# Optimization experiments

Measured on AMD Instinct MI355X. Metric: run time of the kernel, lower is better.

The kernel has to match this reference:

```python
import jax, jax.numpy as jnp
import numpy as np

B, T, N = 512, 1024, 48


def setup_inputs() -> dict:
    key = jax.random.key(0)
    k1, k2, k3, k4 = jax.random.split(key, 4)
    potentials = jax.random.normal(k1, (B, T, N), dtype=jnp.float32)
    y_true = jax.random.randint(k2, (B, T), 0, N, dtype=jnp.int32)
    lengths = jax.random.randint(k3, (B,), 1, T + 1, dtype=jnp.int32)
    transitions = jax.random.normal(k4, (N, N), dtype=jnp.float32)
    return {"potentials": potentials, "y_true": y_true,
            "lengths": lengths, "transitions": transitions}


def _crf_log_likelihood(potentials, tags, lengths, trans):
    # potentials: [B,T,N], tags: [B,T] int, lengths: [B] int, trans: [N,N]
    Bv, Tv, Nv = potentials.shape
    t_idx = jnp.arange(Tv)

    # ---- numerator: score of the given tag sequence ----
    unary = jnp.take_along_axis(potentials, tags[..., None], axis=2)[..., 0]  # [B,T]
    unary_mask = (t_idx[None, :] < lengths[:, None]).astype(potentials.dtype)
    unary_score = jnp.sum(unary * unary_mask, axis=1)  # [B]

    trans_scores = trans[tags[:, :-1], tags[:, 1:]]  # [B,T-1]
    pair_mask = (t_idx[None, 1:] < lengths[:, None]).astype(potentials.dtype)
    binary_score = jnp.sum(trans_scores * pair_mask, axis=1)  # [B]
    seq_score = unary_score + binary_score

    # ---- log partition: forward algorithm with length masking ----
    alpha0 = potentials[:, 0, :]  # [B,N]
    pots_rest = jnp.transpose(potentials[:, 1:, :], (1, 0, 2))  # [T-1,B,N]
    valid = (t_idx[1:, None] < lengths[None, :])  # [T-1,B]

    def step(alpha, inp):
        pot_t, v = inp  # [B,N], [B]
        # logsumexp over previous state: alpha[b,i] + trans[i,j]
        new_alpha = jax.nn.logsumexp(alpha[:, :, None] + trans[None, :, :], axis=1) + pot_t
        alpha = jnp.where(v[:, None], new_alpha, alpha)
        return alpha, None

    alpha_final, _ = jax.lax.scan(step, alpha0, (pots_rest, valid))
    log_norm = jax.nn.logsumexp(alpha_final, axis=-1)  # [B]

    return seq_score - log_norm


def reference(potentials, y_true, lengths, transitions):
    ll = _crf_log_likelihood(potentials, y_true.astype(jnp.int32),
                             lengths.astype(jnp.int32), transitions)
    return -ll  # per-sample NLL, shape [B]
```

## Files before the change

kernel.cpp:

```cpp
#include <hip/hip_runtime.h>
#include <cstdint>
#include <cstddef>

constexpr int Bb = 512;
constexpr int Tt = 1024;
constexpr int Nn = 48;
constexpr int SG = 16;
constexpr int NG = Bb / SG;
constexpr int Cc = 16;
constexpr int Lc = Tt / Cc;
constexpr int Wb = 32;
constexpr int AP = 72;

typedef short bf16x8 __attribute__((ext_vector_type(8)));
typedef float f32x4  __attribute__((ext_vector_type(4)));

__device__ __forceinline__ unsigned short bf16_rne(float x) {
    const unsigned int u = __float_as_uint(x);
    return (unsigned short)((u + 0x7FFFu + ((u >> 16) & 1u)) >> 16);
}
__device__ __forceinline__ float safe_log(float x) {
    return __logf(fmaxf(x, 1e-30f));
}

__launch_bounds__(64)
__global__ void crf_fused(const float* __restrict__ pot,
                          const int*   __restrict__ ytrue,
                          const int*   __restrict__ lengths,
                          const float* __restrict__ trans,
                          float*       __restrict__ out)
{
    __shared__ float trans_lds[Nn * Nn];
    __shared__ __align__(16) unsigned short ab[SG][AP];

    const int lane = threadIdx.x;
    const int ln   = lane & 15;
    const int q    = lane >> 4;
    const int gidx = blockIdx.x >> 4;
    const int c    = blockIdx.x & 15;
    const int s0   = gidx * SG;

    for (int i = lane; i < Nn * Nn; i += 64) trans_lds[i] = trans[i];
    for (int i = lane; i < SG * AP; i += 64) ((unsigned short*)ab)[i] = 0;
    __syncthreads();

    {
        const int    b    = blockIdx.x;
        const int    lenb = lengths[b];
        const int*   yrow = ytrue + (size_t)b * Tt;
        const float* prow = pot + (size_t)b * Tt * Nn;
        float gold = 0.0f;
#pragma unroll
        for (int k = 0; k < Tt / 64; ++k) {
            const int   t    = lane + 64 * k;
            const int   yt   = yrow[t];
            const int   ytm1 = yrow[(t > 0) ? (t - 1) : 0];
            const float u    = prow[(size_t)t * Nn + yt];
            const float tr   = trans_lds[ytm1 * Nn + yt];
            gold += (t < lenb) ? u : 0.0f;
            gold += (t >= 1 && t < lenb) ? tr : 0.0f;
        }
#pragma unroll
        for (int off = 32; off > 0; off >>= 1) gold += __shfl_xor(gold, off);
        if (lane == 0) atomicAdd(&out[b], -gold);
    }

    int len4[4];
#pragma unroll
    for (int r = 0; r < 4; ++r) len4[r] = lengths[s0 + q * 4 + r];
    int lmax = lengths[s0 + ln];
#pragma unroll
    for (int off = 8; off > 0; off >>= 1) {
        const int o = __shfl_xor(lmax, off);
        lmax = (o > lmax) ? o : lmax;
    }

    const int start = (c == 0) ? 1 : c * Lc;
    if (c > 0 && start >= lmax) return;
    const int end = ((c + 1) * Lc < lmax) ? (c + 1) * Lc : lmax;

    bf16x8 Bf[3][2];
#pragma unroll
    for (int nt = 0; nt < 3; ++nt)
#pragma unroll
        for (int kc = 0; kc < 2; ++kc)
#pragma unroll
            for (int d = 0; d < 8; ++d) {
                const int i = kc * 32 + q * 8 + d;
                const int j = nt * 16 + ln;
                const float v = (i < Nn) ? __expf(trans_lds[i * Nn + j]) : 0.0f;
                Bf[nt][kc][d] = (short)bf16_rne(v);
            }

    const float* pbase[4];
#pragma unroll
    for (int r = 0; r < 4; ++r)
        pbase[r] = pot + (size_t)(s0 + q * 4 + r) * (Tt * Nn) + ln;

    const int t0 = (c == 0) ? 1 : (start - Wb);

    float pinit[3][4];
#pragma unroll
    for (int nt = 0; nt < 3; ++nt)
#pragma unroll
        for (int r = 0; r < 4; ++r)
            pinit[nt][r] = pbase[r][(size_t)(t0 - 1) * Nn + nt * 16];

    float sh4[4];
#pragma unroll
    for (int r = 0; r < 4; ++r) sh4[r] = __shfl(pinit[0][r], lane & 48);

    float prev[3][4];
    float gacc[4];
#pragma unroll
    for (int r = 0; r < 4; ++r) gacc[r] = (c == 0) ? sh4[r] : 0.0f;
#pragma unroll
    for (int nt = 0; nt < 3; ++nt)
#pragma unroll
        for (int r = 0; r < 4; ++r) {
            const float v = __expf(pinit[nt][r] - sh4[r]);
            prev[nt][r] = v;
            ab[q * 4 + r][nt * 16 + ln] = bf16_rne(v);
        }
    asm volatile("" ::: "memory");
    bf16x8 A0 = *(const bf16x8*)&ab[ln][q * 8];
    bf16x8 A1 = *(const bf16x8*)&ab[ln][32 + q * 8];
    asm volatile("" ::: "memory");

    float epv[3][4], pn1[3][4], pn2[3][4];
#pragma unroll
    for (int nt = 0; nt < 3; ++nt)
#pragma unroll
        for (int r = 0; r < 4; ++r) {
            epv[nt][r] = __expf(pbase[r][(size_t)t0 * Nn + nt * 16]);
            const int ta = (t0 + 1 < Tt) ? t0 + 1 : Tt - 1;
            const int tb = (t0 + 2 < Tt) ? t0 + 2 : Tt - 1;
            pn1[nt][r] = pbase[r][(size_t)ta * Nn + nt * 16];
            pn2[nt][r] = pbase[r][(size_t)tb * Nn + nt * 16];
        }

    for (int t = t0; t < end; ++t) {
        const bool in_win = (t >= start);
        const int  t3 = (t + 3 < Tt) ? (t + 3) : (Tt - 1);
        float pnew[3][4];
#pragma unroll
        for (int nt = 0; nt < 3; ++nt)
#pragma unroll
            for (int r = 0; r < 4; ++r)
                pnew[nt][r] = pbase[r][(size_t)t3 * Nn + nt * 16];

        f32x4 D[3];
#pragma unroll
        for (int nt = 0; nt < 3; ++nt) {
            f32x4 z = {0.0f, 0.0f, 0.0f, 0.0f};
            D[nt] = __builtin_amdgcn_mfma_f32_16x16x32_bf16(A0, Bf[nt][0], z, 0, 0, 0);
            D[nt] = __builtin_amdgcn_mfma_f32_16x16x32_bf16(A1, Bf[nt][1], D[nt], 0, 0, 0);
        }

        float v[3][4];
#pragma unroll
        for (int nt = 0; nt < 3; ++nt)
#pragma unroll
            for (int r = 0; r < 4; ++r)
                v[nt][r] = D[nt][r] * epv[nt][r];

        float c4[4];
#pragma unroll
        for (int r = 0; r < 4; ++r) c4[r] = __shfl(v[0][r], lane & 48);

        float rr[4];
#pragma unroll
        for (int r = 0; r < 4; ++r) rr[r] = __builtin_amdgcn_rcpf(fmaxf(c4[r], 1e-30f));
#pragma unroll
        for (int r = 0; r < 4; ++r) {
            const float lg = safe_log(c4[r]);
            gacc[r] += (in_win && (t < len4[r])) ? lg : 0.0f;
        }
#pragma unroll
        for (int nt = 0; nt < 3; ++nt)
#pragma unroll
            for (int r = 0; r < 4; ++r) {
                const float ns = (t < len4[r]) ? (v[nt][r] * rr[r]) : prev[nt][r];
                prev[nt][r] = ns;
                ab[q * 4 + r][nt * 16 + ln] = bf16_rne(ns);
            }
        asm volatile("" ::: "memory");
        A0 = *(const bf16x8*)&ab[ln][q * 8];
        A1 = *(const bf16x8*)&ab[ln][32 + q * 8];
        asm volatile("" ::: "memory");

#pragma unroll
        for (int nt = 0; nt < 3; ++nt)
#pragma unroll
            for (int r = 0; r < 4; ++r) {
                epv[nt][r] = __expf(pn1[nt][r]);
                pn1[nt][r] = pn2[nt][r];
                pn2[nt][r] = pnew[nt][r];
            }
    }

    float G[4];
#pragma unroll
    for (int r = 0; r < 4; ++r) {
        float rs = prev[0][r] + prev[1][r] + prev[2][r];
#pragma unroll
        for (int off = 8; off > 0; off >>= 1) rs += __shfl_xor(rs, off);
        const bool active_chunk = (c == 0) || (c * Lc < len4[r]);
        const bool last = active_chunk && (len4[r] <= (c + 1) * Lc);
        const float lgr = safe_log(rs);
        G[r] = gacc[r] + (last ? lgr : 0.0f);
    }
    if (ln == 0) {
#pragma unroll
        for (int r = 0; r < 4; ++r) atomicAdd(&out[s0 + q * 4 + r], G[r]);
    }
}

extern "C" void kernel_launch(void* const* d_in, const int* in_sizes, int n_in,
                              void* d_out, int out_size, void* d_ws, size_t ws_size,
                              hipStream_t stream)
{
    const float* pot   = (const float*)d_in[0];
    const int*   ytrue = (const int*)  d_in[1];
    const int*   lens  = (const int*)  d_in[2];
    const float* trans = (const float*)d_in[3];
    float*       out   = (float*)d_out;

    hipMemsetAsync(out, 0, (size_t)out_size * sizeof(float), stream);
    crf_fused<<<dim3(NG * Cc), dim3(64), 0, stream>>>(pot, ytrue, lens, trans, out);
}
```

Baseline: 210.1 us.

## Double time chunks per sequence group and unroll recurrence with 4-deep prefetch ring

Splits the time axis into 32 chunks instead of 16, so each block runs a shorter serial forward recurrence (32-step window plus 32-step warmup) and the grid doubles to 1024 single-wave blocks. The gold-path score work is split across the two blocks now mapped to each sequence. The inner loop is unrolled by four, with a ring buffer that prefetches potentials four steps ahead, and sched_barrier replaces the asm memory fences. The trade is more total warmup work and atomics, plus padding steps at the end of each chunk, in exchange for shorter critical paths and more parallel waves.

Measured after the change: 195.2 us. 1.08x faster.

```diff
diff --git a/kernel.cpp b/kernel.cpp
--- a/kernel.cpp
+++ b/kernel.cpp
@@ -7,7 +7,7 @@
 constexpr int Nn = 48;
 constexpr int SG = 16;
 constexpr int NG = Bb / SG;
-constexpr int Cc = 16;
+constexpr int Cc = 32;
 constexpr int Lc = Tt / Cc;
 constexpr int Wb = 32;
 constexpr int AP = 72;
@@ -23,7 +23,7 @@
     return __logf(fmaxf(x, 1e-30f));
 }
 
-__launch_bounds__(64)
+__launch_bounds__(64, 1)
 __global__ void crf_fused(const float* __restrict__ pot,
                           const int*   __restrict__ ytrue,
                           const int*   __restrict__ lengths,
@@ -36,8 +36,8 @@
     const int lane = threadIdx.x;
     const int ln   = lane & 15;
     const int q    = lane >> 4;
-    const int gidx = blockIdx.x >> 4;
-    const int c    = blockIdx.x & 15;
+    const int gidx = blockIdx.x >> 5;
+    const int c    = blockIdx.x & 31;
     const int s0   = gidx * SG;
 
     for (int i = lane; i < Nn * Nn; i += 64) trans_lds[i] = trans[i];
@@ -45,14 +45,15 @@
     __syncthreads();
 
     {
-        const int    b    = blockIdx.x;
+        const int    b    = blockIdx.x >> 1;
+        const int    h    = blockIdx.x & 1;
         const int    lenb = lengths[b];
         const int*   yrow = ytrue + (size_t)b * Tt;
         const float* prow = pot + (size_t)b * Tt * Nn;
         float gold = 0.0f;
 #pragma unroll
-        for (int k = 0; k < Tt / 64; ++k) {
-            const int   t    = lane + 64 * k;
+        for (int k = 0; k < Tt / 128; ++k) {
+            const int   t    = h * (Tt / 2) + lane + 64 * k;
             const int   yt   = yrow[t];
             const int   ytm1 = yrow[(t > 0) ? (t - 1) : 0];
             const float u    = prow[(size_t)t * Nn + yt];
@@ -97,7 +98,8 @@
     for (int r = 0; r < 4; ++r)
         pbase[r] = pot + (size_t)(s0 + q * 4 + r) * (Tt * Nn) + ln;
 
-    const int t0 = (c == 0) ? 1 : (start - Wb);
+    int t0 = (c == 0) ? 1 : (start - Wb);
+    if (t0 < 1) t0 = 1;
 
     float pinit[3][4];
 #pragma unroll
@@ -122,82 +124,93 @@
             prev[nt][r] = v;
             ab[q * 4 + r][nt * 16 + ln] = bf16_rne(v);
         }
-    asm volatile("" ::: "memory");
+    __builtin_amdgcn_sched_barrier(0);
     bf16x8 A0 = *(const bf16x8*)&ab[ln][q * 8];
     bf16x8 A1 = *(const bf16x8*)&ab[ln][32 + q * 8];
-    asm volatile("" ::: "memory");
-
-    float epv[3][4], pn1[3][4], pn2[3][4];
-#pragma unroll
-    for (int nt = 0; nt < 3; ++nt)
-#pragma unroll
-        for (int r = 0; r < 4; ++r) {
-            epv[nt][r] = __expf(pbase[r][(size_t)t0 * Nn + nt * 16]);
-            const int ta = (t0 + 1 < Tt) ? t0 + 1 : Tt - 1;
-            const int tb = (t0 + 2 < Tt) ? t0 + 2 : Tt - 1;
-            pn1[nt][r] = pbase[r][(size_t)ta * Nn + nt * 16];
-            pn2[nt][r] = pbase[r][(size_t)tb * Nn + nt * 16];
-        }
-
-    for (int t = t0; t < end; ++t) {
-        const bool in_win = (t >= start);
-        const int  t3 = (t + 3 < Tt) ? (t + 3) : (Tt - 1);
-        float pnew[3][4];
+    __builtin_amdgcn_sched_barrier(0);
+
+    float pbuf[4][3][4];
+#pragma unroll
+    for (int s = 0; s < 4; ++s) {
+        const int ts = (t0 + s < Tt) ? (t0 + s) : (Tt - 1);
 #pragma unroll
         for (int nt = 0; nt < 3; ++nt)
 #pragma unroll
             for (int r = 0; r < 4; ++r)
-                pnew[nt][r] = pbase[r][(size_t)t3 * Nn + nt * 16];
-
-        f32x4 D[3];
-#pragma unroll
-        for (int nt = 0; nt < 3; ++nt) {
-            f32x4 z = {0.0f, 0.0f, 0.0f, 0.0f};
-            D[nt] = __builtin_amdgcn_mfma_f32_16x16x32_bf16(A0, Bf[nt][0], z, 0, 0, 0);
-            D[nt] = __builtin_amdgcn_mfma_f32_16x16x32_bf16(A1, Bf[nt][1], D[nt], 0, 0, 0);
-        }
-
-        float v[3][4];
-#pragma unroll
-        for (int nt = 0; nt < 3; ++nt)
-#pragma unroll
-            for (int r = 0; r < 4; ++r)
-                v[nt][r] = D[nt][r] * epv[nt][r];
-
-        float c4[4];
-#pragma unroll
-        for (int r = 0; r < 4; ++r) c4[r] = __shfl(v[0][r], lane & 48);
-
-        float rr[4];
-#pragma unroll
-        for (int r = 0; r < 4; ++r) rr[r] = __builtin_amdgcn_rcpf(fmaxf(c4[r], 1e-30f));
-#pragma unroll
-        for (int r = 0; r < 4; ++r) {
-            const float lg = safe_log(c4[r]);
-            gacc[r] += (in_win && (t < len4[r])) ? lg : 0.0f;
-        }
-#pragma unroll
-        for (int nt = 0; nt < 3; ++nt)
-#pragma unroll
-            for (int r = 0; r < 4; ++r) {
-                const float ns = (t < len4[r]) ? (v[nt][r] * rr[r]) : prev[nt][r];
-                prev[nt][r] = ns;
-                ab[q * 4 + r][nt * 16 + ln] = bf16_rne(ns);
-            }
-        asm volatile("" ::: "memory");
-        A0 = *(const bf16x8*)&ab[ln][q * 8];
-        A1 = *(const bf16x8*)&ab[ln][32 + q * 8];
-        asm volatile("" ::: "memory");
-
-#pragma unroll
-        for (int nt = 0; nt < 3; ++nt)
-#pragma unroll
-            for (int r = 0; r < 4; ++r) {
-                epv[nt][r] = __expf(pn1[nt][r]);
-                pn1[nt][r] = pn2[nt][r];
-                pn2[nt][r] = pnew[nt][r];
-            }
-    }
+                pbuf[s][nt][r] = pbase[r][(size_t)ts * Nn + nt * 16];
+    }
+    float epv[3][4];
+#pragma unroll
+    for (int nt = 0; nt < 3; ++nt)
+#pragma unroll
+        for (int r = 0; r < 4; ++r)
+            epv[nt][r] = __expf(pbuf[0][nt][r]);
+
+    const int ksteps = ((end - t0) + 3) & ~3;
+
+#define CRF_STEP(KK, SS)                                                        \
+    {                                                                           \
+        const int t   = t0 + (KK);                                              \
+        const int tld = (t + 4 < Tt) ? (t + 4) : (Tt - 1);                      \
+        _Pragma("unroll")                                                       \
+        for (int nt = 0; nt < 3; ++nt) {                                        \
+            _Pragma("unroll")                                                   \
+            for (int r = 0; r < 4; ++r)                                         \
+                pbuf[SS][nt][r] = pbase[r][(size_t)tld * Nn + nt * 16];         \
+        }                                                                       \
+        f32x4 D[3];                                                             \
+        _Pragma("unroll")                                                       \
+        for (int nt = 0; nt < 3; ++nt) {                                        \
+            f32x4 z = {0.0f, 0.0f, 0.0f, 0.0f};                                 \
+            D[nt] = __builtin_amdgcn_mfma_f32_16x16x32_bf16(A0, Bf[nt][0], z, 0, 0, 0); \
+            D[nt] = __builtin_amdgcn_mfma_f32_16x16x32_bf16(A1, Bf[nt][1], D[nt], 0, 0, 0); \
+        }                                                                       \
+        float vv[3][4];                                                         \
+        _Pragma("unroll")                                                       \
+        for (int nt = 0; nt < 3; ++nt) {                                        \
+            _Pragma("unroll")                                                   \
+            for (int r = 0; r < 4; ++r)                                         \
+                vv[nt][r] = D[nt][r] * epv[nt][r];                              \
+        }                                                                       \
+        float c4[4];                                                            \
+        _Pragma("unroll")                                                       \
+        for (int r = 0; r < 4; ++r) c4[r] = __shfl(vv[0][r], lane & 48);        \
+        float rr[4];                                                            \
+        _Pragma("unroll")                                                       \
+        for (int r = 0; r < 4; ++r) rr[r] = __builtin_amdgcn_rcpf(fmaxf(c4[r], 1e-30f)); \
+        _Pragma("unroll")                                                       \
+        for (int r = 0; r < 4; ++r) {                                           \
+            const float lg = safe_log(c4[r]);                                   \
+            gacc[r] += ((t >= start) && (t < len4[r]) && (t < end)) ? lg : 0.0f; \
+        }                                                                       \
+        _Pragma("unroll")                                                       \
+        for (int nt = 0; nt < 3; ++nt) {                                        \
+            _Pragma("unroll")                                                   \
+            for (int r = 0; r < 4; ++r) {                                       \
+                const float ns = (t < len4[r]) ? (vv[nt][r] * rr[r]) : prev[nt][r]; \
+                prev[nt][r] = ns;                                               \
+                ab[q * 4 + r][nt * 16 + ln] = bf16_rne(ns);                     \
+            }                                                                   \
+        }                                                                       \
+        __builtin_amdgcn_sched_barrier(0);                                      \
+        A0 = *(const bf16x8*)&ab[ln][q * 8];                                    \
+        A1 = *(const bf16x8*)&ab[ln][32 + q * 8];                               \
+        __builtin_amdgcn_sched_barrier(0);                                      \
+        _Pragma("unroll")                                                       \
+        for (int nt = 0; nt < 3; ++nt) {                                        \
+            _Pragma("unroll")                                                   \
+            for (int r = 0; r < 4; ++r)                                         \
+                epv[nt][r] = __expf(pbuf[((SS) + 1) & 3][nt][r]);               \
+        }                                                                       \
+    }
+
+    for (int k = 0; k < ksteps; k += 4) {
+        CRF_STEP(k + 0, 0);
+        CRF_STEP(k + 1, 1);
+        CRF_STEP(k + 2, 2);
+        CRF_STEP(k + 3, 3);
+    }
+#undef CRF_STEP
 
     float G[4];
 #pragma unroll
```
